# Kernel optimization log

Measured on AMD Instinct MI355X. Metric: run time of the kernel, lower is better.

Reference implementation:

```python
import jax, jax.numpy as jnp
import numpy as np

HSV_BINS = 32
LBP_BINS = 256
NEG_SLOPE = 0.2
ENV_CLASSES = 4
SEASON_CLASSES = 4


def rgb_to_hsv(img):
    # img: [N, 3, H, W] in [0, 1]
    img = jnp.clip(img, 0.0, 1.0)
    r, g, b = img[:, 0], img[:, 1], img[:, 2]
    maxc = img.max(axis=1)
    minc = img.min(axis=1)
    delta = maxc - minc
    mask = delta > 1e-6
    safe = jnp.where(mask, delta, 1.0)
    hue = jnp.zeros_like(maxc)
    hue = jnp.where((maxc == r) & mask, jnp.mod((g - b) / safe, 6.0), hue)
    hue = jnp.where((maxc == g) & mask, (b - r) / safe + 2.0, hue)
    hue = jnp.where((maxc == b) & mask, (r - g) / safe + 4.0, hue)
    hue = hue / 6.0
    sat = jnp.where(maxc > 1e-6, delta / jnp.maximum(maxc, 1e-6), jnp.zeros_like(maxc))
    return jnp.stack((hue, sat, maxc), axis=1)


def hist_features(hsv):
    # torch.histc(bins=32, min=0, max=1); HSV values are all in [0,1],
    # value==1.0 falls into the last bin -> clip(floor(v*bins), 0, bins-1).
    N, C, H, W = hsv.shape
    v = hsv.reshape(N * C, H * W)
    idx = jnp.clip(jnp.floor(v * HSV_BINS).astype(jnp.int32), 0, HSV_BINS - 1)
    offset = jnp.arange(N * C, dtype=jnp.int32)[:, None] * HSV_BINS
    counts = jnp.bincount((idx + offset).reshape(-1), length=N * C * HSV_BINS)
    counts = counts.reshape(N * C, HSV_BINS).astype(jnp.float32)
    counts = counts / jnp.maximum(counts.sum(-1, keepdims=True), 1.0)
    return counts.reshape(N, C * HSV_BINS)


def lbp_features(hsv):
    N, C, H, W = hsv.shape
    p = jnp.pad(hsv, ((0, 0), (0, 0), (1, 1), (1, 1)), mode='reflect')
    offsets = [(0, 0), (0, 1), (0, 2), (1, 2), (2, 2), (2, 1), (2, 0), (1, 0)]
    codes = jnp.zeros((N, C, H, W), dtype=jnp.int32)
    for bit, (dy, dx) in enumerate(offsets):
        nb = jax.lax.dynamic_slice(p, (0, 0, dy, dx), (N, C, H, W))
        codes = codes + (nb >= hsv).astype(jnp.int32) * (1 << bit)
    codes = codes.reshape(N * C, H * W)
    offset = jnp.arange(N * C, dtype=jnp.int32)[:, None] * LBP_BINS
    counts = jnp.bincount((codes + offset).reshape(-1), length=N * C * LBP_BINS)
    counts = counts.reshape(N * C, LBP_BINS).astype(jnp.float32)
    counts = counts / jnp.maximum(counts.sum(-1, keepdims=True), 1.0)
    return counts.reshape(N, C * LBP_BINS)


def setup_inputs() -> dict:
    key = jax.random.key(0)
    k1, k2, k3, k4, k5 = jax.random.split(key, 5)
    B, T, H, W = 4, 8, 512, 512
    sequence = jax.random.uniform(k1, (B, T, 3, H, W), dtype=jnp.float32)
    high = jax.random.normal(k2, (B * T, 2048), dtype=jnp.float32)
    Wp = jax.random.normal(k3, (512, 2912), dtype=jnp.float32) * 0.02
    bp = jnp.zeros((512,), dtype=jnp.float32)
    environment_id = jax.random.randint(k4, (B,), 0, ENV_CLASSES, dtype=jnp.int64 if jax.config.jax_enable_x64 else jnp.int32)
    season_id = jax.random.randint(k5, (B,), 0, SEASON_CLASSES, dtype=jnp.int64 if jax.config.jax_enable_x64 else jnp.int32)
    return {"sequence": sequence, "high": high, "W": Wp, "b": bp,
            "environment_id": environment_id, "season_id": season_id}


def reference(sequence, high, W, b, environment_id, season_id):
    B, T, C, H, Wd = sequence.shape
    # inputs are already in [0,1) so _to_unit_rgb reduces to a clamp
    frames = jnp.clip(sequence, 0.0, 1.0).reshape(B * T, C, H, Wd)
    hsv = rgb_to_hsv(frames)                                   # [BT,3,H,W]
    low = jnp.concatenate((hist_features(hsv), lbp_features(hsv)), axis=1)  # [BT,864]
    fused = jnp.concatenate((high, low), axis=1).reshape(B, T, -1)          # [B,T,2912]
    aggregated = fused.mean(axis=1)                             # [B,2912]
    z = aggregated @ W.T + b                                    # Linear(2912->512)
    c_feat = jnp.where(z >= 0, z, NEG_SLOPE * z)                # LeakyReLU(0.2)
    env = jax.nn.one_hot(environment_id, ENV_CLASSES, dtype=jnp.float32)
    season = jax.nn.one_hot(season_id, SEASON_CLASSES, dtype=jnp.float32)
    c_cls = jnp.concatenate((env, season), axis=1)
    return (c_feat, c_cls)
```

## Files before the change

kernel.cpp:

```cpp
#include <hip/hip_runtime.h>

#define IMH 512
#define IMW 512
#define NFRAMES 32
#define HSV_BINS 32
#define LBP_BINS 256
#define FEAT_HIGH 2048
#define FEAT_LOW (3*HSV_BINS + 3*LBP_BINS)
#define FEAT_TOT (FEAT_HIGH + FEAT_LOW)
#define OUT_COLS 512
#define R_ROWS 2
#define STRIPS (IMH / (4 * R_ROWS))
#define NHREP 16
#define NLREP 4

__device__ __forceinline__ void rgb2hsv(float r, float g, float b,
                                        float& h, float& s, float& v) {
    float maxc = fmaxf(r, fmaxf(g, b));
    float minc = fminf(r, fminf(g, b));
    float delta = maxc - minc;
    bool mask = delta > 1e-6f;
    float rd = __builtin_amdgcn_rcpf(mask ? delta : 1.0f);
    float hue = 0.0f;
    if (mask) {
        if (maxc == r) { float t = (g - b) * rd; hue = (t >= 0.0f) ? t : t + 6.0f; }
        if (maxc == g) hue = (b - r) * rd + 2.0f;
        if (maxc == b) hue = (r - g) * rd + 4.0f;
    }
    h = hue * (1.0f / 6.0f);
    s = (maxc > 1e-6f) ? delta * __builtin_amdgcn_rcpf(maxc) : 0.0f;
    v = maxc;
}

__device__ __forceinline__ void loadcvt_row(const float* __restrict__ base, int gy,
                                            int x0, int lane,
                                            float (&h)[10], float (&s)[10], float (&v)[10]) {
    const float* p0 = base + (size_t)gy * IMW + x0;
    float4 ra = *(const float4*)(p0);
    float4 rb = *(const float4*)(p0 + 4);
    float4 ga = *(const float4*)(p0 + IMH * IMW);
    float4 gb = *(const float4*)(p0 + IMH * IMW + 4);
    float4 ba = *(const float4*)(p0 + 2 * IMH * IMW);
    float4 bb = *(const float4*)(p0 + 2 * IMH * IMW + 4);
    rgb2hsv(ra.x, ga.x, ba.x, h[1], s[1], v[1]);
    rgb2hsv(ra.y, ga.y, ba.y, h[2], s[2], v[2]);
    rgb2hsv(ra.z, ga.z, ba.z, h[3], s[3], v[3]);
    rgb2hsv(ra.w, ga.w, ba.w, h[4], s[4], v[4]);
    rgb2hsv(rb.x, gb.x, bb.x, h[5], s[5], v[5]);
    rgb2hsv(rb.y, gb.y, bb.y, h[6], s[6], v[6]);
    rgb2hsv(rb.z, gb.z, bb.z, h[7], s[7], v[7]);
    rgb2hsv(rb.w, gb.w, bb.w, h[8], s[8], v[8]);
    float hl = __shfl(h[8], (lane + 63) & 63);
    float sl = __shfl(s[8], (lane + 63) & 63);
    float vl = __shfl(v[8], (lane + 63) & 63);
    float hr = __shfl(h[1], (lane + 1) & 63);
    float sr = __shfl(s[1], (lane + 1) & 63);
    float vr = __shfl(v[1], (lane + 1) & 63);
    h[0] = (lane == 0) ? h[2] : hl;
    s[0] = (lane == 0) ? s[2] : sl;
    v[0] = (lane == 0) ? v[2] : vl;
    h[9] = (lane == 63) ? h[7] : hr;
    s[9] = (lane == 63) ? s[7] : sr;
    v[9] = (lane == 63) ? v[7] : vr;
}

__device__ __forceinline__ void emit_ch(const float (&u)[10], const float (&c)[10],
                                        const float (&d)[10],
                                        unsigned* __restrict__ hb, unsigned* __restrict__ lb) {
#pragma unroll
    for (int j = 0; j < 8; ++j) {
        float ce = c[j + 1];
        int code = 0;
        code |= (u[j]     >= ce) ? 1   : 0;
        code |= (u[j + 1] >= ce) ? 2   : 0;
        code |= (u[j + 2] >= ce) ? 4   : 0;
        code |= (c[j + 2] >= ce) ? 8   : 0;
        code |= (d[j + 2] >= ce) ? 16  : 0;
        code |= (d[j + 1] >= ce) ? 32  : 0;
        code |= (d[j]     >= ce) ? 64  : 0;
        code |= (c[j]     >= ce) ? 128 : 0;
        int bin = min((int)(ce * 32.0f), HSV_BINS - 1);
        atomicAdd(hb + bin, 1u);
        atomicAdd(lb + code, 1u);
    }
}

__global__ __launch_bounds__(256, 4) void hist_lbp_kernel(const float* __restrict__ seq,
                                                          unsigned* __restrict__ hist_g,
                                                          unsigned* __restrict__ lbp_g) {
    const int n     = blockIdx.x >> 6;
    const int strip = blockIdx.x & (STRIPS - 1);
    const int tid   = threadIdx.x;
    const int lane  = tid & 63;
    const int w     = tid >> 6;
    const int x0    = lane << 3;
    const int yb    = strip * (4 * R_ROWS) + w * R_ROWS;

    __shared__ unsigned sh_hist[3][NHREP][HSV_BINS + 1];
    __shared__ unsigned sh_lbp[3][NLREP][LBP_BINS + 1];

    for (int i = tid; i < 3 * NHREP * (HSV_BINS + 1); i += 256) ((unsigned*)sh_hist)[i] = 0u;
    for (int i = tid; i < 3 * NLREP * (LBP_BINS + 1); i += 256) ((unsigned*)sh_lbp)[i] = 0u;
    __syncthreads();

    unsigned* hb0 = &sh_hist[0][lane & (NHREP - 1)][0];
    unsigned* hb1 = &sh_hist[1][lane & (NHREP - 1)][0];
    unsigned* hb2 = &sh_hist[2][lane & (NHREP - 1)][0];
    unsigned* lb0 = &sh_lbp[0][lane & (NLREP - 1)][0];
    unsigned* lb1 = &sh_lbp[1][lane & (NLREP - 1)][0];
    unsigned* lb2 = &sh_lbp[2][lane & (NLREP - 1)][0];

    const float* base = seq + (size_t)n * 3 * IMH * IMW;

    float Ah[10], As[10], Av[10];
    float Bh[10], Bs[10], Bv[10];
    float Ch[10], Cs[10], Cv[10];

    const int ytop = (yb == 0) ? 1 : yb - 1;
    const int ybot = (yb + R_ROWS == IMH) ? IMH - 2 : yb + R_ROWS;

    loadcvt_row(base, ytop,   x0, lane, Ah, As, Av);
    loadcvt_row(base, yb,     x0, lane, Bh, Bs, Bv);

    loadcvt_row(base, yb + 1, x0, lane, Ch, Cs, Cv);
    emit_ch(Ah, Bh, Ch, hb0, lb0);
    emit_ch(As, Bs, Cs, hb1, lb1);
    emit_ch(Av, Bv, Cv, hb2, lb2);

    loadcvt_row(base, ybot,   x0, lane, Ah, As, Av);
    emit_ch(Bh, Ch, Ah, hb0, lb0);
    emit_ch(Bs, Cs, As, hb1, lb1);
    emit_ch(Bv, Cv, Av, hb2, lb2);

    __syncthreads();
    for (int i = tid; i < 3 * HSV_BINS; i += 256) {
        int c = i >> 5, b = i & 31;
        unsigned s = 0;
#pragma unroll
        for (int r = 0; r < NHREP; ++r) s += sh_hist[c][r][b];
        if (s) atomicAdd(&hist_g[n * 3 * HSV_BINS + i], s);
    }
    for (int i = tid; i < 3 * LBP_BINS; i += 256) {
        int c = i >> 8, b = i & 255;
        unsigned s = 0;
#pragma unroll
        for (int r = 0; r < NLREP; ++r) s += sh_lbp[c][r][b];
        if (s) atomicAdd(&lbp_g[n * 3 * LBP_BINS + i], s);
    }
}

__global__ __launch_bounds__(256) void agg_cls_kernel(const float* __restrict__ high,
                                                      const unsigned* __restrict__ hist_g,
                                                      const unsigned* __restrict__ lbp_g,
                                                      const int* __restrict__ env,
                                                      const int* __restrict__ season,
                                                      float* __restrict__ agg,
                                                      float* __restrict__ out) {
    int idx = blockIdx.x * blockDim.x + threadIdx.x;
    if (idx >= 4 * FEAT_TOT + 32) return;
    if (idx >= 4 * FEAT_TOT) {
        int t = idx - 4 * FEAT_TOT;
        int i = t >> 3;
        int p = t & 7;
        float v;
        if (p < 4) v = (env[i] == p) ? 1.0f : 0.0f;
        else       v = (season[i] == p - 4) ? 1.0f : 0.0f;
        out[4 * OUT_COLS + t] = v;
        return;
    }
    int bb = idx / FEAT_TOT;
    int k  = idx % FEAT_TOT;
    float s = 0.0f;
    const float inv = 1.0f / 262144.0f;
    if (k < FEAT_HIGH) {
#pragma unroll
        for (int t = 0; t < 8; t++) s += high[(size_t)(bb * 8 + t) * FEAT_HIGH + k];
    } else if (k < FEAT_HIGH + 3 * HSV_BINS) {
        int f = k - FEAT_HIGH;
#pragma unroll
        for (int t = 0; t < 8; t++)
            s += (float)hist_g[(bb * 8 + t) * 3 * HSV_BINS + f] * inv;
    } else {
        int f = k - FEAT_HIGH - 3 * HSV_BINS;
#pragma unroll
        for (int t = 0; t < 8; t++)
            s += (float)lbp_g[(bb * 8 + t) * 3 * LBP_BINS + f] * inv;
    }
    agg[idx] = s * 0.125f;
}

__global__ __launch_bounds__(256) void gemm_kernel(const float* __restrict__ agg,
                                                   const float* __restrict__ Wm,
                                                   const float* __restrict__ bias,
                                                   float* __restrict__ out) {
    const int j = blockIdx.x;
    const int tid = threadIdx.x;
    const float* wrow = Wm + (size_t)j * FEAT_TOT;
    float a0 = 0.f, a1 = 0.f, a2 = 0.f, a3 = 0.f;
    for (int k = tid; k < FEAT_TOT; k += 256) {
        float w = wrow[k];
        a0 += agg[k] * w;
        a1 += agg[FEAT_TOT + k] * w;
        a2 += agg[2 * FEAT_TOT + k] * w;
        a3 += agg[3 * FEAT_TOT + k] * w;
    }
#pragma unroll
    for (int off = 32; off > 0; off >>= 1) {
        a0 += __shfl_down(a0, off);
        a1 += __shfl_down(a1, off);
        a2 += __shfl_down(a2, off);
        a3 += __shfl_down(a3, off);
    }
    __shared__ float red[4][4];
    if ((tid & 63) == 0) {
        int w = tid >> 6;
        red[w][0] = a0; red[w][1] = a1; red[w][2] = a2; red[w][3] = a3;
    }
    __syncthreads();
    if (tid < 4) {
        float z = red[0][tid] + red[1][tid] + red[2][tid] + red[3][tid] + bias[j];
        out[tid * OUT_COLS + j] = (z >= 0.0f) ? z : 0.2f * z;
    }
}

extern "C" void kernel_launch(void* const* d_in, const int* in_sizes, int n_in,
                              void* d_out, int out_size, void* d_ws, size_t ws_size,
                              hipStream_t stream) {
    const float* seq    = (const float*)d_in[0];
    const float* high   = (const float*)d_in[1];
    const float* Wm     = (const float*)d_in[2];
    const float* bias   = (const float*)d_in[3];
    const int*   env    = (const int*)d_in[4];
    const int*   season = (const int*)d_in[5];
    float* out = (float*)d_out;

    unsigned* hist_g = (unsigned*)d_ws;
    unsigned* lbp_g  = hist_g + NFRAMES * 3 * HSV_BINS;
    float*    agg    = (float*)(lbp_g + NFRAMES * 3 * LBP_BINS);

    size_t histBytes = (size_t)(NFRAMES * 3 * HSV_BINS + NFRAMES * 3 * LBP_BINS) * sizeof(unsigned);
    hipMemsetAsync(d_ws, 0, histBytes, stream);

    hist_lbp_kernel<<<NFRAMES * STRIPS, 256, 0, stream>>>(seq, hist_g, lbp_g);
    agg_cls_kernel<<<(4 * FEAT_TOT + 32 + 255) / 256, 256, 0, stream>>>(high, hist_g, lbp_g, env, season, agg, out);
    gemm_kernel<<<OUT_COLS, 256, 0, stream>>>(agg, Wm, bias, out);
}
```

Before: 182.7 us.

## Use packed 16-bit per-lane shared histograms with larger blocks and XCD-aware block mapping

Replaces the few shared-memory histogram replicas with per-lane (hist) and per-32-lane (LBP) private sub-histograms, packing two 16-bit bins per 32-bit word so the replicas fit in LDS. This aims to remove atomic contention on shared bins. It also raises the block to 1024 threads covering 32 rows, which quarters the number of blocks and global flushes, and remaps block IDs so neighbouring strips of the same frame are spread across XCDs. In exchange the final reduction has to walk 64 or 32 columns per bin, and the 16-bit counters could overflow if a replica ever received 65536 or more hits.

New measurement: 197.5 us. +8.1%, slower.

```diff
diff --git a/kernel.cpp b/kernel.cpp
--- a/kernel.cpp
+++ b/kernel.cpp
@@ -9,10 +9,8 @@
 #define FEAT_LOW (3*HSV_BINS + 3*LBP_BINS)
 #define FEAT_TOT (FEAT_HIGH + FEAT_LOW)
 #define OUT_COLS 512
-#define R_ROWS 2
-#define STRIPS (IMH / (4 * R_ROWS))
-#define NHREP 16
-#define NLREP 4
+#define BROWS 32
+#define STRIPS (IMH / BROWS)
 
 __device__ __forceinline__ void rgb2hsv(float r, float g, float b,
                                         float& h, float& s, float& v) {
@@ -80,35 +78,37 @@
         code |= (d[j]     >= ce) ? 64  : 0;
         code |= (c[j]     >= ce) ? 128 : 0;
         int bin = min((int)(ce * 32.0f), HSV_BINS - 1);
-        atomicAdd(hb + bin, 1u);
-        atomicAdd(lb + code, 1u);
-    }
-}
-
-__global__ __launch_bounds__(256, 4) void hist_lbp_kernel(const float* __restrict__ seq,
-                                                          unsigned* __restrict__ hist_g,
-                                                          unsigned* __restrict__ lbp_g) {
-    const int n     = blockIdx.x >> 6;
-    const int strip = blockIdx.x & (STRIPS - 1);
+        atomicAdd(hb + ((bin >> 1) << 6), 1u << ((bin & 1) << 4));
+        atomicAdd(lb + ((code >> 1) << 5), 1u << ((code & 1) << 4));
+    }
+}
+
+__global__ __launch_bounds__(1024, 4) void hist_lbp_kernel(const float* __restrict__ seq,
+                                                           unsigned* __restrict__ hist_g,
+                                                           unsigned* __restrict__ lbp_g) {
+    const int bid     = blockIdx.x;
+    const int logical = ((bid & 7) << 6) | (bid >> 3);
+    const int n     = logical >> 4;
+    const int strip = logical & (STRIPS - 1);
     const int tid   = threadIdx.x;
     const int lane  = tid & 63;
     const int w     = tid >> 6;
     const int x0    = lane << 3;
-    const int yb    = strip * (4 * R_ROWS) + w * R_ROWS;
-
-    __shared__ unsigned sh_hist[3][NHREP][HSV_BINS + 1];
-    __shared__ unsigned sh_lbp[3][NLREP][LBP_BINS + 1];
-
-    for (int i = tid; i < 3 * NHREP * (HSV_BINS + 1); i += 256) ((unsigned*)sh_hist)[i] = 0u;
-    for (int i = tid; i < 3 * NLREP * (LBP_BINS + 1); i += 256) ((unsigned*)sh_lbp)[i] = 0u;
+    const int yb    = strip * BROWS + w * 2;
+
+    __shared__ unsigned sh_hist[3][HSV_BINS / 2][64];
+    __shared__ unsigned sh_lbp[3][LBP_BINS / 2][32];
+
+    for (int i = tid; i < 3 * (HSV_BINS / 2) * 64; i += 1024) ((unsigned*)sh_hist)[i] = 0u;
+    for (int i = tid; i < 3 * (LBP_BINS / 2) * 32; i += 1024) ((unsigned*)sh_lbp)[i] = 0u;
     __syncthreads();
 
-    unsigned* hb0 = &sh_hist[0][lane & (NHREP - 1)][0];
-    unsigned* hb1 = &sh_hist[1][lane & (NHREP - 1)][0];
-    unsigned* hb2 = &sh_hist[2][lane & (NHREP - 1)][0];
-    unsigned* lb0 = &sh_lbp[0][lane & (NLREP - 1)][0];
-    unsigned* lb1 = &sh_lbp[1][lane & (NLREP - 1)][0];
-    unsigned* lb2 = &sh_lbp[2][lane & (NLREP - 1)][0];
+    unsigned* hb0 = &sh_hist[0][0][lane];
+    unsigned* hb1 = &sh_hist[1][0][lane];
+    unsigned* hb2 = &sh_hist[2][0][lane];
+    unsigned* lb0 = &sh_lbp[0][0][lane & 31];
+    unsigned* lb1 = &sh_lbp[1][0][lane & 31];
+    unsigned* lb2 = &sh_lbp[2][0][lane & 31];
 
     const float* base = seq + (size_t)n * 3 * IMH * IMW;
 
@@ -117,7 +117,7 @@
     float Ch[10], Cs[10], Cv[10];
 
     const int ytop = (yb == 0) ? 1 : yb - 1;
-    const int ybot = (yb + R_ROWS == IMH) ? IMH - 2 : yb + R_ROWS;
+    const int ybot = (yb + 2 == IMH) ? IMH - 2 : yb + 2;
 
     loadcvt_row(base, ytop,   x0, lane, Ah, As, Av);
     loadcvt_row(base, yb,     x0, lane, Bh, Bs, Bv);
@@ -133,19 +133,29 @@
     emit_ch(Bv, Cv, Av, hb2, lb2);
 
     __syncthreads();
-    for (int i = tid; i < 3 * HSV_BINS; i += 256) {
-        int c = i >> 5, b = i & 31;
+    if (tid < 3 * HSV_BINS) {
+        int c = tid >> 5, b = tid & 31;
+        const unsigned* row = &sh_hist[c][b >> 1][0];
+        int sh = (b & 1) << 4;
         unsigned s = 0;
 #pragma unroll
-        for (int r = 0; r < NHREP; ++r) s += sh_hist[c][r][b];
-        if (s) atomicAdd(&hist_g[n * 3 * HSV_BINS + i], s);
-    }
-    for (int i = tid; i < 3 * LBP_BINS; i += 256) {
-        int c = i >> 8, b = i & 255;
+        for (int j = 0; j < 64; ++j) {
+            int col = (tid + j) & 63;
+            s += (row[col] >> sh) & 0xFFFFu;
+        }
+        if (s) atomicAdd(&hist_g[n * 3 * HSV_BINS + tid], s);
+    }
+    if (tid < 3 * LBP_BINS) {
+        int c = tid >> 8, code = tid & 255;
+        const unsigned* row = &sh_lbp[c][code >> 1][0];
+        int sh = (code & 1) << 4;
         unsigned s = 0;
 #pragma unroll
-        for (int r = 0; r < NLREP; ++r) s += sh_lbp[c][r][b];
-        if (s) atomicAdd(&lbp_g[n * 3 * LBP_BINS + i], s);
+        for (int j = 0; j < 32; ++j) {
+            int col = (tid + j) & 31;
+            s += (row[col] >> sh) & 0xFFFFu;
+        }
+        if (s) atomicAdd(&lbp_g[n * 3 * LBP_BINS + tid], s);
     }
 }
 
@@ -241,7 +251,7 @@
     size_t histBytes = (size_t)(NFRAMES * 3 * HSV_BINS + NFRAMES * 3 * LBP_BINS) * sizeof(unsigned);
     hipMemsetAsync(d_ws, 0, histBytes, stream);
 
-    hist_lbp_kernel<<<NFRAMES * STRIPS, 256, 0, stream>>>(seq, hist_g, lbp_g);
+    hist_lbp_kernel<<<NFRAMES * STRIPS, 1024, 0, stream>>>(seq, hist_g, lbp_g);
     agg_cls_kernel<<<(4 * FEAT_TOT + 32 + 255) / 256, 256, 0, stream>>>(high, hist_g, lbp_g, env, season, agg, out);
     gemm_kernel<<<OUT_COLS, 256, 0, stream>>>(agg, Wm, bias, out);
 }
```

## Process four rows per wave with a rolling HSV window and prefetched raw loads

Applied to the files above, without the earlier changes.

Each wave now handles four image rows instead of two, keeping a rotating three-row window of converted HSV values. This cuts the share of halo rows that are loaded and converted twice, and halves the number of blocks, so there is less shared-histogram setup and fewer global atomic flushes. The global load for the next row is split from its conversion so it can be issued before the current row's histogram atomics, overlapping memory latency with LDS work. The cost is higher register pressure and fewer blocks to fill the GPU, and the launch grid elsewhere must match the new strip count.

New measurement: 185.7 us. About the same (+1.6%).

```diff
diff --git a/kernel.cpp b/kernel.cpp
--- a/kernel.cpp
+++ b/kernel.cpp
@@ -9,8 +9,9 @@
 #define FEAT_LOW (3*HSV_BINS + 3*LBP_BINS)
 #define FEAT_TOT (FEAT_HIGH + FEAT_LOW)
 #define OUT_COLS 512
-#define R_ROWS 2
-#define STRIPS (IMH / (4 * R_ROWS))
+#define WROWS 4
+#define BROWS (4 * WROWS)
+#define STRIPS (IMH / BROWS)
 #define NHREP 16
 #define NLREP 4
 
@@ -32,24 +33,29 @@
     v = maxc;
 }
 
-__device__ __forceinline__ void loadcvt_row(const float* __restrict__ base, int gy,
-                                            int x0, int lane,
-                                            float (&h)[10], float (&s)[10], float (&v)[10]) {
+struct Raw { float4 ra, rb, ga, gb, ba, bb; };
+
+__device__ __forceinline__ void load_raw(const float* __restrict__ base, int gy,
+                                         int x0, Raw& r) {
     const float* p0 = base + (size_t)gy * IMW + x0;
-    float4 ra = *(const float4*)(p0);
-    float4 rb = *(const float4*)(p0 + 4);
-    float4 ga = *(const float4*)(p0 + IMH * IMW);
-    float4 gb = *(const float4*)(p0 + IMH * IMW + 4);
-    float4 ba = *(const float4*)(p0 + 2 * IMH * IMW);
-    float4 bb = *(const float4*)(p0 + 2 * IMH * IMW + 4);
-    rgb2hsv(ra.x, ga.x, ba.x, h[1], s[1], v[1]);
-    rgb2hsv(ra.y, ga.y, ba.y, h[2], s[2], v[2]);
-    rgb2hsv(ra.z, ga.z, ba.z, h[3], s[3], v[3]);
-    rgb2hsv(ra.w, ga.w, ba.w, h[4], s[4], v[4]);
-    rgb2hsv(rb.x, gb.x, bb.x, h[5], s[5], v[5]);
-    rgb2hsv(rb.y, gb.y, bb.y, h[6], s[6], v[6]);
-    rgb2hsv(rb.z, gb.z, bb.z, h[7], s[7], v[7]);
-    rgb2hsv(rb.w, gb.w, bb.w, h[8], s[8], v[8]);
+    r.ra = *(const float4*)(p0);
+    r.rb = *(const float4*)(p0 + 4);
+    r.ga = *(const float4*)(p0 + IMH * IMW);
+    r.gb = *(const float4*)(p0 + IMH * IMW + 4);
+    r.ba = *(const float4*)(p0 + 2 * IMH * IMW);
+    r.bb = *(const float4*)(p0 + 2 * IMH * IMW + 4);
+}
+
+__device__ __forceinline__ void cvt_row(const Raw& r, int lane,
+                                        float (&h)[10], float (&s)[10], float (&v)[10]) {
+    rgb2hsv(r.ra.x, r.ga.x, r.ba.x, h[1], s[1], v[1]);
+    rgb2hsv(r.ra.y, r.ga.y, r.ba.y, h[2], s[2], v[2]);
+    rgb2hsv(r.ra.z, r.ga.z, r.ba.z, h[3], s[3], v[3]);
+    rgb2hsv(r.ra.w, r.ga.w, r.ba.w, h[4], s[4], v[4]);
+    rgb2hsv(r.rb.x, r.gb.x, r.bb.x, h[5], s[5], v[5]);
+    rgb2hsv(r.rb.y, r.gb.y, r.bb.y, h[6], s[6], v[6]);
+    rgb2hsv(r.rb.z, r.gb.z, r.bb.z, h[7], s[7], v[7]);
+    rgb2hsv(r.rb.w, r.gb.w, r.bb.w, h[8], s[8], v[8]);
     float hl = __shfl(h[8], (lane + 63) & 63);
     float sl = __shfl(s[8], (lane + 63) & 63);
     float vl = __shfl(v[8], (lane + 63) & 63);
@@ -88,13 +94,14 @@
 __global__ __launch_bounds__(256, 4) void hist_lbp_kernel(const float* __restrict__ seq,
                                                           unsigned* __restrict__ hist_g,
                                                           unsigned* __restrict__ lbp_g) {
-    const int n     = blockIdx.x >> 6;
-    const int strip = blockIdx.x & (STRIPS - 1);
+    const int bid   = blockIdx.x;
+    const int n     = bid >> 5;
+    const int strip = bid & (STRIPS - 1);
     const int tid   = threadIdx.x;
     const int lane  = tid & 63;
     const int w     = tid >> 6;
     const int x0    = lane << 3;
-    const int yb    = strip * (4 * R_ROWS) + w * R_ROWS;
+    const int yb    = strip * BROWS + w * WROWS;
 
     __shared__ unsigned sh_hist[3][NHREP][HSV_BINS + 1];
     __shared__ unsigned sh_lbp[3][NLREP][LBP_BINS + 1];
@@ -112,25 +119,28 @@
 
     const float* base = seq + (size_t)n * 3 * IMH * IMW;
 
-    float Ah[10], As[10], Av[10];
-    float Bh[10], Bs[10], Bv[10];
-    float Ch[10], Cs[10], Cv[10];
+    float Wh[3][10], Ws[3][10], Wv[3][10];
+    Raw raw0, raw1;
 
     const int ytop = (yb == 0) ? 1 : yb - 1;
-    const int ybot = (yb + R_ROWS == IMH) ? IMH - 2 : yb + R_ROWS;
-
-    loadcvt_row(base, ytop,   x0, lane, Ah, As, Av);
-    loadcvt_row(base, yb,     x0, lane, Bh, Bs, Bv);
-
-    loadcvt_row(base, yb + 1, x0, lane, Ch, Cs, Cv);
-    emit_ch(Ah, Bh, Ch, hb0, lb0);
-    emit_ch(As, Bs, Cs, hb1, lb1);
-    emit_ch(Av, Bv, Cv, hb2, lb2);
-
-    loadcvt_row(base, ybot,   x0, lane, Ah, As, Av);
-    emit_ch(Bh, Ch, Ah, hb0, lb0);
-    emit_ch(Bs, Cs, As, hb1, lb1);
-    emit_ch(Bv, Cv, Av, hb2, lb2);
+    load_raw(base, ytop,   x0, raw0);
+    load_raw(base, yb,     x0, raw1);
+    cvt_row(raw0, lane, Wh[0], Ws[0], Wv[0]);
+    load_raw(base, yb + 1, x0, raw0);
+    cvt_row(raw1, lane, Wh[1], Ws[1], Wv[1]);
+
+#pragma unroll
+    for (int i = 0; i < WROWS; ++i) {
+        cvt_row(raw0, lane, Wh[(2 + i) % 3], Ws[(2 + i) % 3], Wv[(2 + i) % 3]);
+        if (i < WROWS - 1) {
+            int ri = yb + 2 + i;
+            if (ri == IMH) ri = IMH - 2;
+            load_raw(base, ri, x0, raw0);
+        }
+        emit_ch(Wh[i % 3], Wh[(1 + i) % 3], Wh[(2 + i) % 3], hb0, lb0);
+        emit_ch(Ws[i % 3], Ws[(1 + i) % 3], Ws[(2 + i) % 3], hb1, lb1);
+        emit_ch(Wv[i % 3], Wv[(1 + i) % 3], Wv[(2 + i) % 3], hb2, lb2);
+    }
 
     __syncthreads();
     for (int i = tid; i < 3 * HSV_BINS; i += 256) {
```

## Restructure histogram/LBP kernel to one pixel per lane with vertical row streaming

Applied to the files above, without the earlier changes.

The work mapping changes from each lane handling 8 horizontal pixels over 2 rows to each lane handling one column pixel while walking a 16-row strip. A rolling three-row register window lets each converted row be reused vertically, so halo rows are re-converted far less often than with 2-row strips. The next row's loads are prefetched ahead of the emit work. In exchange, global loads become scalar rather than float4, the edge lanes issue extra gathers and HSV conversions for horizontal halos, and the grid shape changes to 32 strips times 2 halves per frame.

Result: no change. 180.6 us (-1.2%).

```diff
diff --git a/kernel.cpp b/kernel.cpp
--- a/kernel.cpp
+++ b/kernel.cpp
@@ -9,8 +9,9 @@
 #define FEAT_LOW (3*HSV_BINS + 3*LBP_BINS)
 #define FEAT_TOT (FEAT_HIGH + FEAT_LOW)
 #define OUT_COLS 512
-#define R_ROWS 2
-#define STRIPS (IMH / (4 * R_ROWS))
+#define RSTRIP 16
+#define STRIPS (IMH / RSTRIP)
+#define HALVES 2
 #define NHREP 16
 #define NLREP 4
 
@@ -32,69 +33,64 @@
     v = maxc;
 }
 
-__device__ __forceinline__ void loadcvt_row(const float* __restrict__ base, int gy,
-                                            int x0, int lane,
-                                            float (&h)[10], float (&s)[10], float (&v)[10]) {
-    const float* p0 = base + (size_t)gy * IMW + x0;
-    float4 ra = *(const float4*)(p0);
-    float4 rb = *(const float4*)(p0 + 4);
-    float4 ga = *(const float4*)(p0 + IMH * IMW);
-    float4 gb = *(const float4*)(p0 + IMH * IMW + 4);
-    float4 ba = *(const float4*)(p0 + 2 * IMH * IMW);
-    float4 bb = *(const float4*)(p0 + 2 * IMH * IMW + 4);
-    rgb2hsv(ra.x, ga.x, ba.x, h[1], s[1], v[1]);
-    rgb2hsv(ra.y, ga.y, ba.y, h[2], s[2], v[2]);
-    rgb2hsv(ra.z, ga.z, ba.z, h[3], s[3], v[3]);
-    rgb2hsv(ra.w, ga.w, ba.w, h[4], s[4], v[4]);
-    rgb2hsv(rb.x, gb.x, bb.x, h[5], s[5], v[5]);
-    rgb2hsv(rb.y, gb.y, bb.y, h[6], s[6], v[6]);
-    rgb2hsv(rb.z, gb.z, bb.z, h[7], s[7], v[7]);
-    rgb2hsv(rb.w, gb.w, bb.w, h[8], s[8], v[8]);
-    float hl = __shfl(h[8], (lane + 63) & 63);
-    float sl = __shfl(s[8], (lane + 63) & 63);
-    float vl = __shfl(v[8], (lane + 63) & 63);
-    float hr = __shfl(h[1], (lane + 1) & 63);
-    float sr = __shfl(s[1], (lane + 1) & 63);
-    float vr = __shfl(v[1], (lane + 1) & 63);
-    h[0] = (lane == 0) ? h[2] : hl;
-    s[0] = (lane == 0) ? s[2] : sl;
-    v[0] = (lane == 0) ? v[2] : vl;
-    h[9] = (lane == 63) ? h[7] : hr;
-    s[9] = (lane == 63) ? s[7] : sr;
-    v[9] = (lane == 63) ? v[7] : vr;
-}
-
-__device__ __forceinline__ void emit_ch(const float (&u)[10], const float (&c)[10],
-                                        const float (&d)[10],
-                                        unsigned* __restrict__ hb, unsigned* __restrict__ lb) {
-#pragma unroll
-    for (int j = 0; j < 8; ++j) {
-        float ce = c[j + 1];
-        int code = 0;
-        code |= (u[j]     >= ce) ? 1   : 0;
-        code |= (u[j + 1] >= ce) ? 2   : 0;
-        code |= (u[j + 2] >= ce) ? 4   : 0;
-        code |= (c[j + 2] >= ce) ? 8   : 0;
-        code |= (d[j + 2] >= ce) ? 16  : 0;
-        code |= (d[j + 1] >= ce) ? 32  : 0;
-        code |= (d[j]     >= ce) ? 64  : 0;
-        code |= (c[j]     >= ce) ? 128 : 0;
-        int bin = min((int)(ce * 32.0f), HSV_BINS - 1);
-        atomicAdd(hb + bin, 1u);
-        atomicAdd(lb + code, 1u);
-    }
+struct Row { float hl, hc, hr, sl, sc, sr, vl, vc, vr; };
+
+__device__ __forceinline__ void cvt_shfl(const float* __restrict__ pR,
+                                         const float* __restrict__ pG,
+                                         const float* __restrict__ pB,
+                                         int ry, int x, int lane,
+                                         float r, float g, float b, Row& o) {
+    rgb2hsv(r, g, b, o.hc, o.sc, o.vc);
+    o.hl = __shfl(o.hc, (lane + 63) & 63);
+    o.sl = __shfl(o.sc, (lane + 63) & 63);
+    o.vl = __shfl(o.vc, (lane + 63) & 63);
+    o.hr = __shfl(o.hc, (lane + 1) & 63);
+    o.sr = __shfl(o.sc, (lane + 1) & 63);
+    o.vr = __shfl(o.vc, (lane + 1) & 63);
+    if (lane == 0 || lane == 63) {
+        int xe = (lane == 0) ? x - 1 : x + 1;
+        if (xe < 0) xe = 1;
+        if (xe > IMW - 1) xe = IMW - 2;
+        size_t eo = (size_t)ry * IMW + xe;
+        float he, se, ve;
+        rgb2hsv(pR[eo], pG[eo], pB[eo], he, se, ve);
+        if (lane == 0) { o.hl = he; o.sl = se; o.vl = ve; }
+        else           { o.hr = he; o.sr = se; o.vr = ve; }
+    }
+}
+
+__device__ __forceinline__ void emit1(float ul, float uc, float ur,
+                                      float cl, float ce, float cr,
+                                      float dl, float dc, float dr,
+                                      unsigned* __restrict__ hb,
+                                      unsigned* __restrict__ lb) {
+    int code = 0;
+    code |= (ul >= ce) ? 1   : 0;
+    code |= (uc >= ce) ? 2   : 0;
+    code |= (ur >= ce) ? 4   : 0;
+    code |= (cr >= ce) ? 8   : 0;
+    code |= (dr >= ce) ? 16  : 0;
+    code |= (dc >= ce) ? 32  : 0;
+    code |= (dl >= ce) ? 64  : 0;
+    code |= (cl >= ce) ? 128 : 0;
+    int bin = min((int)(ce * 32.0f), HSV_BINS - 1);
+    atomicAdd(hb + bin, 1u);
+    atomicAdd(lb + code, 1u);
 }
 
 __global__ __launch_bounds__(256, 4) void hist_lbp_kernel(const float* __restrict__ seq,
                                                           unsigned* __restrict__ hist_g,
                                                           unsigned* __restrict__ lbp_g) {
-    const int n     = blockIdx.x >> 6;
-    const int strip = blockIdx.x & (STRIPS - 1);
+    const int bid   = blockIdx.x;
+    const int n     = bid >> 6;
+    const int rem   = bid & 63;
+    const int strip = rem >> 1;
+    const int half  = rem & 1;
     const int tid   = threadIdx.x;
     const int lane  = tid & 63;
     const int w     = tid >> 6;
-    const int x0    = lane << 3;
-    const int yb    = strip * (4 * R_ROWS) + w * R_ROWS;
+    const int x     = half * 256 + w * 64 + lane;
+    const int yb    = strip * RSTRIP;
 
     __shared__ unsigned sh_hist[3][NHREP][HSV_BINS + 1];
     __shared__ unsigned sh_lbp[3][NLREP][LBP_BINS + 1];
@@ -110,27 +106,40 @@
     unsigned* lb1 = &sh_lbp[1][lane & (NLREP - 1)][0];
     unsigned* lb2 = &sh_lbp[2][lane & (NLREP - 1)][0];
 
-    const float* base = seq + (size_t)n * 3 * IMH * IMW;
-
-    float Ah[10], As[10], Av[10];
-    float Bh[10], Bs[10], Bv[10];
-    float Ch[10], Cs[10], Cv[10];
-
+    const float* pR = seq + (size_t)n * 3 * IMH * IMW;
+    const float* pG = pR + (size_t)IMH * IMW;
+    const float* pB = pR + 2 * (size_t)IMH * IMW;
+
+    Row U, C, D;
     const int ytop = (yb == 0) ? 1 : yb - 1;
-    const int ybot = (yb + R_ROWS == IMH) ? IMH - 2 : yb + R_ROWS;
-
-    loadcvt_row(base, ytop,   x0, lane, Ah, As, Av);
-    loadcvt_row(base, yb,     x0, lane, Bh, Bs, Bv);
-
-    loadcvt_row(base, yb + 1, x0, lane, Ch, Cs, Cv);
-    emit_ch(Ah, Bh, Ch, hb0, lb0);
-    emit_ch(As, Bs, Cs, hb1, lb1);
-    emit_ch(Av, Bv, Cv, hb2, lb2);
-
-    loadcvt_row(base, ybot,   x0, lane, Ah, As, Av);
-    emit_ch(Bh, Ch, Ah, hb0, lb0);
-    emit_ch(Bs, Cs, As, hb1, lb1);
-    emit_ch(Bv, Cv, Av, hb2, lb2);
+    {
+        size_t o = (size_t)ytop * IMW + x;
+        cvt_shfl(pR, pG, pB, ytop, x, lane, pR[o], pG[o], pB[o], U);
+        o = (size_t)yb * IMW + x;
+        cvt_shfl(pR, pG, pB, yb, x, lane, pR[o], pG[o], pB[o], C);
+    }
+    float rn, gn, bn;
+    {
+        size_t o = (size_t)(yb + 1) * IMW + x;
+        rn = pR[o]; gn = pG[o]; bn = pB[o];
+    }
+
+#pragma unroll 2
+    for (int i = 0; i < RSTRIP; ++i) {
+        int ry = yb + 1 + i;
+        if (ry == IMH) ry = IMH - 2;
+        cvt_shfl(pR, pG, pB, ry, x, lane, rn, gn, bn, D);
+        if (i < RSTRIP - 1) {
+            int r2 = yb + 2 + i;
+            if (r2 == IMH) r2 = IMH - 2;
+            size_t o = (size_t)r2 * IMW + x;
+            rn = pR[o]; gn = pG[o]; bn = pB[o];
+        }
+        emit1(U.hl, U.hc, U.hr, C.hl, C.hc, C.hr, D.hl, D.hc, D.hr, hb0, lb0);
+        emit1(U.sl, U.sc, U.sr, C.sl, C.sc, C.sr, D.sl, D.sc, D.sr, hb1, lb1);
+        emit1(U.vl, U.vc, U.vr, C.vl, C.vc, C.vr, D.vl, D.vc, D.vr, hb2, lb2);
+        U = C; C = D;
+    }
 
     __syncthreads();
     for (int i = tid; i < 3 * HSV_BINS; i += 256) {
@@ -241,7 +250,7 @@
     size_t histBytes = (size_t)(NFRAMES * 3 * HSV_BINS + NFRAMES * 3 * LBP_BINS) * sizeof(unsigned);
     hipMemsetAsync(d_ws, 0, histBytes, stream);
 
-    hist_lbp_kernel<<<NFRAMES * STRIPS, 256, 0, stream>>>(seq, hist_g, lbp_g);
+    hist_lbp_kernel<<<NFRAMES * STRIPS * HALVES, 256, 0, stream>>>(seq, hist_g, lbp_g);
     agg_cls_kernel<<<(4 * FEAT_TOT + 32 + 255) / 256, 256, 0, stream>>>(high, hist_g, lbp_g, env, season, agg, out);
     gemm_kernel<<<OUT_COLS, 256, 0, stream>>>(agg, Wm, bias, out);
 }
```
